# Optimization experiments

Measured on AMD Instinct MI355X. Metric: run time of the kernel, lower is better.

## Reference

```python
import jax, jax.numpy as jnp
import numpy as np

M, K, N = 4096, 4096, 11008  # tokens, in_features, out_features


def setup_inputs() -> dict:
    key = jax.random.key(0)
    k0, k1, k2 = jax.random.split(key, 3)
    # quint8 activations: values in [0, 255], zero_point 128
    x_q = jax.random.randint(k0, (M, K), 0, 256, dtype=jnp.int32)
    # qint8 weight: values in [-128, 127], zero_point 0 (as prepacked in __init__)
    w_q = jax.random.randint(k1, (N, K), -128, 128, dtype=jnp.int32)
    bias = jax.random.normal(k2, (N,), dtype=jnp.float32) * 0.1
    return {
        "x_q": x_q,
        "w_q": w_q,
        "bias": bias,
        "x_scale": jnp.float32(0.02),
        "w_scale": jnp.float32(0.01),
        "out_scale": jnp.float32(1.0),   # self.scale = 1.0
        "x_zero_point": 128,
        "out_zero_point": 0,             # self.zero_point = 0
    }


def reference(x_q, w_q, bias, x_scale, w_scale, out_scale, x_zero_point, out_zero_point):
    # int8 GEMM with int32 accumulation: (x - zp_x) @ W^T
    acc = jnp.einsum(
        "mk,nk->mn",
        x_q - x_zero_point,
        w_q,
        preferred_element_type=jnp.int32,
    )
    # dequantize + bias (fp32), then requantize to quint8 output
    y = acc.astype(jnp.float32) * (x_scale * w_scale) + bias
    q = jnp.clip(jnp.round(y / out_scale) + out_zero_point, 0, 255).astype(jnp.int32)
    return q
```

## Files before the change

### kernel.cpp

```cpp
#include <hip/hip_runtime.h>

#define M_DIM 4096
#define K_DIM 4096
#define N_DIM 11008
#define BM 256
#define BN 256
#define BK 64
#define NTILES (K_DIM / BK)

typedef int v4i  __attribute__((ext_vector_type(4)));
typedef int v16i __attribute__((ext_vector_type(16)));

#define WAIT_VM8 0x3F78
#define WAIT_VM0 0x3F70

__device__ __forceinline__ void load_lds16(const void* g, void* l) {
    __builtin_amdgcn_global_load_lds(
        (const __attribute__((address_space(1))) void*)g,
        (__attribute__((address_space(3))) void*)l,
        16, 0, 0);
}

__global__ void pack_x_kernel(const int* __restrict__ x, signed char* __restrict__ out,
                              const int* __restrict__ zp_p, int n4) {
    int i = blockIdx.x * blockDim.x + threadIdx.x;
    if (i >= n4) return;
    int zp = zp_p[0];
    int4 v = ((const int4*)x)[i];
    unsigned int p = ((unsigned int)(v.x - zp) & 0xFF)
                   | (((unsigned int)(v.y - zp) & 0xFF) << 8)
                   | (((unsigned int)(v.z - zp) & 0xFF) << 16)
                   | (((unsigned int)(v.w - zp) & 0xFF) << 24);
    ((unsigned int*)out)[i] = p;
}

__global__ void pack_w_kernel(const int* __restrict__ w, signed char* __restrict__ out, int n4) {
    int i = blockIdx.x * blockDim.x + threadIdx.x;
    if (i >= n4) return;
    int4 v = ((const int4*)w)[i];
    unsigned int p = ((unsigned int)v.x & 0xFF)
                   | (((unsigned int)v.y & 0xFF) << 8)
                   | (((unsigned int)v.z & 0xFF) << 16)
                   | (((unsigned int)v.w & 0xFF) << 24);
    ((unsigned int*)out)[i] = p;
}

__global__ __launch_bounds__(256, 1) void gemm_i8_kernel(
    const signed char* __restrict__ A8,
    const signed char* __restrict__ B8,
    const float* __restrict__ bias,
    const float* __restrict__ xs_p, const float* __restrict__ ws_p,
    const float* __restrict__ os_p, const int* __restrict__ ozp_p,
    int* __restrict__ out) {
    __shared__ v4i As0[BM * BK / 16];
    __shared__ v4i Bs0[BN * BK / 16];
    __shared__ v4i As1[BM * BK / 16];
    __shared__ v4i Bs1[BN * BK / 16];

    const int tid  = threadIdx.x;
    const int lane = tid & 63;
    const int wave = tid >> 6;

    const int bid   = blockIdx.x;
    const int xcd   = bid & 7;
    const int local = bid >> 3;
    const int m_blk = xcd * 2 + (local & 1);
    const int n_blk = local >> 1;
    const int m0 = m_blk * BM;
    const int n0 = n_blk * BN;

    int offA[4], offB[4], ldsSlot[4];
#pragma unroll
    for (int j = 0; j < 4; ++j) {
        const int s   = tid + 256 * j;
        const int row = s >> 2;
        const int gg  = (s & 3) ^ ((row >> 1) & 3);
        offA[j]    = (m0 + row) * K_DIM + gg * 16;
        offB[j]    = (n0 + row) * K_DIM + gg * 16;
        ldsSlot[j] = s;
    }

    const int waveM = wave >> 1, waveN = wave & 1;
    const int l31 = lane & 31, h = lane >> 5;
    int aSlot[4][2], bSlot[4][2];
#pragma unroll
    for (int t = 0; t < 4; ++t) {
        const int rA = waveM * 128 + t * 32 + l31;
        const int rB = waveN * 128 + t * 32 + l31;
#pragma unroll
        for (int s = 0; s < 2; ++s) {
            const int g = 2 * s + h;
            aSlot[t][s] = rA * 4 + (g ^ ((rA >> 1) & 3));
            bSlot[t][s] = rB * 4 + (g ^ ((rB >> 1) & 3));
        }
    }

    v16i acc[4][4];
#pragma unroll
    for (int mt = 0; mt < 4; ++mt)
#pragma unroll
        for (int nt = 0; nt < 4; ++nt)
#pragma unroll
            for (int r = 0; r < 16; ++r) acc[mt][nt][r] = 0;

    auto stage = [&](int tile, v4i* Asb, v4i* Bsb) {
        const int koff = tile * BK;
#pragma unroll
        for (int j = 0; j < 4; ++j) load_lds16(A8 + offA[j] + koff, (char*)(Asb + ldsSlot[j]));
#pragma unroll
        for (int j = 0; j < 4; ++j) load_lds16(B8 + offB[j] + koff, (char*)(Bsb + ldsSlot[j]));
    };
    auto compute = [&](const v4i* Asb, const v4i* Bsb) {
#pragma unroll
        for (int s = 0; s < 2; ++s) {
            v4i a[4], b[4];
#pragma unroll
            for (int t = 0; t < 4; ++t) a[t] = Asb[aSlot[t][s]];
#pragma unroll
            for (int t = 0; t < 4; ++t) b[t] = Bsb[bSlot[t][s]];
#pragma unroll
            for (int mt = 0; mt < 4; ++mt)
#pragma unroll
                for (int nt = 0; nt < 4; ++nt)
                    acc[mt][nt] = __builtin_amdgcn_mfma_i32_32x32x32_i8(
                        a[mt], b[nt], acc[mt][nt], 0, 0, 0);
        }
    };

    stage(0, As0, Bs0);
    stage(1, As1, Bs1);

#pragma unroll 1
    for (int kk = 0; kk < NTILES / 2 - 1; ++kk) {
        const int k = 2 * kk;
        __builtin_amdgcn_s_waitcnt(WAIT_VM8);
        __builtin_amdgcn_s_barrier();
        compute(As0, Bs0);
        __builtin_amdgcn_s_barrier();
        stage(k + 2, As0, Bs0);
        __builtin_amdgcn_s_waitcnt(WAIT_VM8);
        __builtin_amdgcn_s_barrier();
        compute(As1, Bs1);
        __builtin_amdgcn_s_barrier();
        stage(k + 3, As1, Bs1);
    }
    __builtin_amdgcn_s_waitcnt(WAIT_VM8);
    __builtin_amdgcn_s_barrier();
    compute(As0, Bs0);
    __builtin_amdgcn_s_waitcnt(WAIT_VM0);
    __builtin_amdgcn_s_barrier();
    compute(As1, Bs1);

    const float scale  = xs_p[0] * ws_p[0];
    const float inv_os = 1.0f / os_p[0];
    const int   ozp    = ozp_p[0];
#pragma unroll
    for (int mt = 0; mt < 4; ++mt) {
        const int rbase = m0 + waveM * 128 + mt * 32 + 4 * h;
#pragma unroll
        for (int nt = 0; nt < 4; ++nt) {
            const int col = n0 + waveN * 128 + nt * 32 + l31;
            const float bv = bias[col];
#pragma unroll
            for (int r = 0; r < 16; ++r) {
                const int row = rbase + (r & 3) + 8 * (r >> 2);
                float y = (float)acc[mt][nt][r] * scale + bv;
                int q = (int)rintf(y * inv_os) + ozp;
                q = q < 0 ? 0 : (q > 255 ? 255 : q);
                out[(long)row * N_DIM + col] = q;
            }
        }
    }
}

extern "C" void kernel_launch(void* const* d_in, const int* in_sizes, int n_in,
                              void* d_out, int out_size, void* d_ws, size_t ws_size,
                              hipStream_t stream) {
    const int*   x_q  = (const int*)d_in[0];
    const int*   w_q  = (const int*)d_in[1];
    const float* bias = (const float*)d_in[2];
    const float* xs   = (const float*)d_in[3];
    const float* wsc  = (const float*)d_in[4];
    const float* os   = (const float*)d_in[5];
    const int*   xzp  = (const int*)d_in[6];
    const int*   ozp  = (const int*)d_in[7];

    signed char* x8 = (signed char*)d_ws;
    signed char* w8 = (signed char*)d_ws + (size_t)M_DIM * K_DIM;

    const int nx4 = M_DIM * K_DIM / 4;
    pack_x_kernel<<<(nx4 + 255) / 256, 256, 0, stream>>>(x_q, x8, xzp, nx4);
    const int nw4 = N_DIM * K_DIM / 4;
    pack_w_kernel<<<(nw4 + 255) / 256, 256, 0, stream>>>(w_q, w8, nw4);

    const int nblocks = (M_DIM / BM) * (N_DIM / BN);
    gemm_i8_kernel<<<nblocks, 256, 0, stream>>>(x8, w8, bias, xs, wsc, os, ozp, (int*)d_out);
}
```

Before: 520.0 us.

## Halve GEMM M-tile to allow two blocks per CU and widen pack stores

Reduces the GEMM block tile from 256x256 to 128x256, halving accumulator registers and LDS so two blocks can reside per CU (launch bounds 256,2). The wait count, load mapping and XCD-aware block swizzle are adjusted to match. The pack kernels now process 16 elements per thread and write 16-byte stores. The trade-off is less data reuse per block and more global traffic for B, in exchange for better latency hiding and a finer grid.

```diff
diff --git a/kernel.cpp b/kernel.cpp
--- a/kernel.cpp
+++ b/kernel.cpp
@@ -3,7 +3,7 @@
 #define M_DIM 4096
 #define K_DIM 4096
 #define N_DIM 11008
-#define BM 256
+#define BM 128
 #define BN 256
 #define BK 64
 #define NTILES (K_DIM / BK)
@@ -11,7 +11,7 @@
 typedef int v4i  __attribute__((ext_vector_type(4)));
 typedef int v16i __attribute__((ext_vector_type(16)));
 
-#define WAIT_VM8 0x3F78
+#define WAIT_VM6 0x3F76
 #define WAIT_VM0 0x3F70
 
 __device__ __forceinline__ void load_lds16(const void* g, void* l) {
@@ -22,30 +22,40 @@
 }
 
 __global__ void pack_x_kernel(const int* __restrict__ x, signed char* __restrict__ out,
-                              const int* __restrict__ zp_p, int n4) {
+                              const int* __restrict__ zp_p, int n16) {
     int i = blockIdx.x * blockDim.x + threadIdx.x;
-    if (i >= n4) return;
-    int zp = zp_p[0];
-    int4 v = ((const int4*)x)[i];
-    unsigned int p = ((unsigned int)(v.x - zp) & 0xFF)
-                   | (((unsigned int)(v.y - zp) & 0xFF) << 8)
-                   | (((unsigned int)(v.z - zp) & 0xFF) << 16)
-                   | (((unsigned int)(v.w - zp) & 0xFF) << 24);
-    ((unsigned int*)out)[i] = p;
-}
-
-__global__ void pack_w_kernel(const int* __restrict__ w, signed char* __restrict__ out, int n4) {
+    if (i >= n16) return;
+    const int zp = zp_p[0];
+    unsigned int r[4];
+#pragma unroll
+    for (int j = 0; j < 4; ++j) {
+        int4 v = ((const int4*)x)[i * 4 + j];
+        r[j] = ((unsigned int)(v.x - zp) & 0xFF)
+             | (((unsigned int)(v.y - zp) & 0xFF) << 8)
+             | (((unsigned int)(v.z - zp) & 0xFF) << 16)
+             | (((unsigned int)(v.w - zp) & 0xFF) << 24);
+    }
+    uint4 p = {r[0], r[1], r[2], r[3]};
+    ((uint4*)out)[i] = p;
+}
+
+__global__ void pack_w_kernel(const int* __restrict__ w, signed char* __restrict__ out, int n16) {
     int i = blockIdx.x * blockDim.x + threadIdx.x;
-    if (i >= n4) return;
-    int4 v = ((const int4*)w)[i];
-    unsigned int p = ((unsigned int)v.x & 0xFF)
-                   | (((unsigned int)v.y & 0xFF) << 8)
-                   | (((unsigned int)v.z & 0xFF) << 16)
-                   | (((unsigned int)v.w & 0xFF) << 24);
-    ((unsigned int*)out)[i] = p;
-}
-
-__global__ __launch_bounds__(256, 1) void gemm_i8_kernel(
+    if (i >= n16) return;
+    unsigned int r[4];
+#pragma unroll
+    for (int j = 0; j < 4; ++j) {
+        int4 v = ((const int4*)w)[i * 4 + j];
+        r[j] = ((unsigned int)v.x & 0xFF)
+             | (((unsigned int)v.y & 0xFF) << 8)
+             | (((unsigned int)v.z & 0xFF) << 16)
+             | (((unsigned int)v.w & 0xFF) << 24);
+    }
+    uint4 p = {r[0], r[1], r[2], r[3]};
+    ((uint4*)out)[i] = p;
+}
+
+__global__ __launch_bounds__(256, 2) void gemm_i8_kernel(
     const signed char* __restrict__ A8,
     const signed char* __restrict__ B8,
     const float* __restrict__ bias,
@@ -64,40 +74,55 @@
     const int bid   = blockIdx.x;
     const int xcd   = bid & 7;
     const int local = bid >> 3;
-    const int m_blk = xcd * 2 + (local & 1);
-    const int n_blk = local >> 1;
+    const int m_blk = xcd * 4 + (local & 3);
+    const int n_blk = local >> 2;
     const int m0 = m_blk * BM;
     const int n0 = n_blk * BN;
 
-    int offA[4], offB[4], ldsSlot[4];
+    int offA[2], ldsSlotA[2];
+#pragma unroll
+    for (int j = 0; j < 2; ++j) {
+        const int s   = tid + 256 * j;
+        const int row = s >> 2;
+        const int gg  = (s & 3) ^ ((row >> 1) & 3);
+        offA[j]     = (m0 + row) * K_DIM + gg * 16;
+        ldsSlotA[j] = s;
+    }
+    int offB[4], ldsSlotB[4];
 #pragma unroll
     for (int j = 0; j < 4; ++j) {
         const int s   = tid + 256 * j;
         const int row = s >> 2;
         const int gg  = (s & 3) ^ ((row >> 1) & 3);
-        offA[j]    = (m0 + row) * K_DIM + gg * 16;
-        offB[j]    = (n0 + row) * K_DIM + gg * 16;
-        ldsSlot[j] = s;
+        offB[j]     = (n0 + row) * K_DIM + gg * 16;
+        ldsSlotB[j] = s;
     }
 
     const int waveM = wave >> 1, waveN = wave & 1;
     const int l31 = lane & 31, h = lane >> 5;
-    int aSlot[4][2], bSlot[4][2];
-#pragma unroll
-    for (int t = 0; t < 4; ++t) {
-        const int rA = waveM * 128 + t * 32 + l31;
-        const int rB = waveN * 128 + t * 32 + l31;
-#pragma unroll
-        for (int s = 0; s < 2; ++s) {
-            const int g = 2 * s + h;
-            aSlot[t][s] = rA * 4 + (g ^ ((rA >> 1) & 3));
-            bSlot[t][s] = rB * 4 + (g ^ ((rB >> 1) & 3));
-        }
-    }
-
-    v16i acc[4][4];
-#pragma unroll
-    for (int mt = 0; mt < 4; ++mt)
+    int aSlot[2][2], bSlot[4][2];
+#pragma unroll
+    for (int t = 0; t < 2; ++t) {
+        const int rA = waveM * 64 + t * 32 + l31;
+#pragma unroll
+        for (int ks = 0; ks < 2; ++ks) {
+            const int g = ks * 2 + h;
+            aSlot[t][ks] = rA * 4 + (g ^ ((rA >> 1) & 3));
+        }
+    }
+#pragma unroll
+    for (int u = 0; u < 4; ++u) {
+        const int rB = waveN * 128 + u * 32 + l31;
+#pragma unroll
+        for (int ks = 0; ks < 2; ++ks) {
+            const int g = ks * 2 + h;
+            bSlot[u][ks] = rB * 4 + (g ^ ((rB >> 1) & 3));
+        }
+    }
+
+    v16i acc[2][4];
+#pragma unroll
+    for (int mt = 0; mt < 2; ++mt)
 #pragma unroll
         for (int nt = 0; nt < 4; ++nt)
 #pragma unroll
@@ -106,20 +131,20 @@
     auto stage = [&](int tile, v4i* Asb, v4i* Bsb) {
         const int koff = tile * BK;
 #pragma unroll
-        for (int j = 0; j < 4; ++j) load_lds16(A8 + offA[j] + koff, (char*)(Asb + ldsSlot[j]));
-#pragma unroll
-        for (int j = 0; j < 4; ++j) load_lds16(B8 + offB[j] + koff, (char*)(Bsb + ldsSlot[j]));
+        for (int j = 0; j < 2; ++j) load_lds16(A8 + offA[j] + koff, (char*)(Asb + ldsSlotA[j]));
+#pragma unroll
+        for (int j = 0; j < 4; ++j) load_lds16(B8 + offB[j] + koff, (char*)(Bsb + ldsSlotB[j]));
     };
     auto compute = [&](const v4i* Asb, const v4i* Bsb) {
 #pragma unroll
-        for (int s = 0; s < 2; ++s) {
-            v4i a[4], b[4];
-#pragma unroll
-            for (int t = 0; t < 4; ++t) a[t] = Asb[aSlot[t][s]];
-#pragma unroll
-            for (int t = 0; t < 4; ++t) b[t] = Bsb[bSlot[t][s]];
-#pragma unroll
-            for (int mt = 0; mt < 4; ++mt)
+        for (int ks = 0; ks < 2; ++ks) {
+            v4i a[2], b[4];
+#pragma unroll
+            for (int t = 0; t < 2; ++t) a[t] = Asb[aSlot[t][ks]];
+#pragma unroll
+            for (int u = 0; u < 4; ++u) b[u] = Bsb[bSlot[u][ks]];
+#pragma unroll
+            for (int mt = 0; mt < 2; ++mt)
 #pragma unroll
                 for (int nt = 0; nt < 4; ++nt)
                     acc[mt][nt] = __builtin_amdgcn_mfma_i32_32x32x32_i8(
@@ -133,18 +158,18 @@
 #pragma unroll 1
     for (int kk = 0; kk < NTILES / 2 - 1; ++kk) {
         const int k = 2 * kk;
-        __builtin_amdgcn_s_waitcnt(WAIT_VM8);
+        __builtin_amdgcn_s_waitcnt(WAIT_VM6);
         __builtin_amdgcn_s_barrier();
         compute(As0, Bs0);
         __builtin_amdgcn_s_barrier();
         stage(k + 2, As0, Bs0);
-        __builtin_amdgcn_s_waitcnt(WAIT_VM8);
+        __builtin_amdgcn_s_waitcnt(WAIT_VM6);
         __builtin_amdgcn_s_barrier();
         compute(As1, Bs1);
         __builtin_amdgcn_s_barrier();
         stage(k + 3, As1, Bs1);
     }
-    __builtin_amdgcn_s_waitcnt(WAIT_VM8);
+    __builtin_amdgcn_s_waitcnt(WAIT_VM6);
     __builtin_amdgcn_s_barrier();
     compute(As0, Bs0);
     __builtin_amdgcn_s_waitcnt(WAIT_VM0);
@@ -155,8 +180,8 @@
     const float inv_os = 1.0f / os_p[0];
     const int   ozp    = ozp_p[0];
 #pragma unroll
-    for (int mt = 0; mt < 4; ++mt) {
-        const int rbase = m0 + waveM * 128 + mt * 32 + 4 * h;
+    for (int mt = 0; mt < 2; ++mt) {
+        const int rbase = m0 + waveM * 64 + mt * 32 + 4 * h;
 #pragma unroll
         for (int nt = 0; nt < 4; ++nt) {
             const int col = n0 + waveN * 128 + nt * 32 + l31;
@@ -188,10 +213,10 @@
     signed char* x8 = (signed char*)d_ws;
     signed char* w8 = (signed char*)d_ws + (size_t)M_DIM * K_DIM;
 
-    const int nx4 = M_DIM * K_DIM / 4;
-    pack_x_kernel<<<(nx4 + 255) / 256, 256, 0, stream>>>(x_q, x8, xzp, nx4);
-    const int nw4 = N_DIM * K_DIM / 4;
-    pack_w_kernel<<<(nw4 + 255) / 256, 256, 0, stream>>>(w_q, w8, nw4);
+    const int nx16 = M_DIM * K_DIM / 16;
+    pack_x_kernel<<<(nx16 + 255) / 256, 256, 0, stream>>>(x_q, x8, xzp, nx16);
+    const int nw16 = N_DIM * K_DIM / 16;
+    pack_w_kernel<<<(nw16 + 255) / 256, 256, 0, stream>>>(w_q, w8, nw16);
 
     const int nblocks = (M_DIM / BM) * (N_DIM / BN);
     gemm_i8_kernel<<<nblocks, 256, 0, stream>>>(x8, w8, bias, xs, wsc, os, ozp, (int*)d_out);
```

Result: slower. 534.3 us (+2.7%).
